# Optimization experiments

Measured on AMD Instinct MI355X. Metric: run time of the kernel, lower is better.

## Reference

```python
import jax, jax.numpy as jnp
import numpy as np
from jax.scipy.special import gammaln

N_NODES = 50000
N_EDGES = 1600000
IN_DIM, H1, H2 = 512, 256, 129  # H2 = hid_dims[-1] + 1 (kappa column)


def setup_inputs() -> dict:
    key = jax.random.key(0)
    k1, k2, k3, k4 = jax.random.split(key, 4)
    x = jax.random.normal(k1, (N_NODES, IN_DIM), dtype=jnp.float32)
    edge_index = jax.random.randint(k2, (2, N_EDGES), 0, N_NODES, dtype=jnp.int32)
    # Glorot-ish init for GCN weights
    W0 = jax.random.normal(k3, (IN_DIM, H1), dtype=jnp.float32) * (1.0 / np.sqrt(IN_DIM))
    W1 = jax.random.normal(k4, (H1, H2), dtype=jnp.float32) * (1.0 / np.sqrt(H1))
    return {"x": x, "edge_index": edge_index, "W0": W0, "W1": W1}


def _gcn_conv(h, W, src, dst, norm, n):
    # PyG GCNConv (bias=False): h' = D^-1/2 (A+I) D^-1/2 (h W)
    h = h @ W
    msg = h[src] * norm[:, None]          # [E+N, F_out]
    return jax.ops.segment_sum(msg, dst, num_segments=n)


def reference(x, edge_index, W0, W1):
    n = x.shape[0]
    loops = jnp.arange(n, dtype=edge_index.dtype)
    src = jnp.concatenate([edge_index[0], loops])
    dst = jnp.concatenate([edge_index[1], loops])
    # symmetric normalization with self-loops (deg >= 1, so rsqrt is safe)
    deg = jax.ops.segment_sum(jnp.ones_like(dst, dtype=x.dtype), dst, num_segments=n)
    dinv = jax.lax.rsqrt(deg)
    norm = dinv[src] * dinv[dst]          # [E+N]

    h = jax.nn.softplus(_gcn_conv(x, W0, src, dst, norm, n))
    # dropout is identity in eval mode (training=False)
    h = jax.nn.softplus(_gcn_conv(h, W1, src, dst, norm, n))

    lbd = h[:, :-1]                       # [N, 128] Weibull scale
    kappa = h[:, -1:] + 0.1               # [N, 1]   Weibull shape
    # deterministic (non-random-encoder / eval) reparameterization:
    # z = lbd * exp(lgamma(1 + 1/kappa))  == E[Weibull(lbd, kappa)]
    z = lbd * jnp.exp(gammaln(1.0 + 1.0 / kappa))
    return z, lbd, kappa
```

## Files before the change

### kernel.cpp

```cpp
#include <hip/hip_runtime.h>
#include <hip/hip_bf16.h>
#include <math.h>


typedef unsigned short ushort_t;
typedef __attribute__((ext_vector_type(8))) short bf16x8;
typedef __attribute__((ext_vector_type(4))) float f32x4;

__device__ __forceinline__ ushort_t f2bf(float f) {
    union { float f; unsigned u; } x; x.f = f;
    unsigned r = x.u + 0x7FFF + ((x.u >> 16) & 1);
    return (ushort_t)(r >> 16);
}
__device__ __forceinline__ float bf2f(ushort_t s) {
    union { unsigned u; float f; } x; x.u = ((unsigned)s) << 16; return x.f;
}

__device__ __forceinline__ void async_copy16(const void* gsrc, void* ldst) {
    __builtin_amdgcn_global_load_lds(
        (const __attribute__((address_space(1))) unsigned int*)gsrc,
        (__attribute__((address_space(3))) unsigned int*)ldst,
        16, 0, 0);
}


__global__ __launch_bounds__(256) void count_kernel(const int* __restrict__ dst,
                                                    int* __restrict__ cnt, int E)
{
    int e = blockIdx.x * blockDim.x + threadIdx.x;
    if (e < E) atomicAdd(&cnt[dst[e]], 1);
}

__global__ __launch_bounds__(1024) void scan_local(const int* __restrict__ cnt,
                                                   int* __restrict__ rowptr,
                                                   float* __restrict__ dinv,
                                                   int* __restrict__ blksum, int N)
{
    __shared__ int wsum[16];
    int tid = threadIdx.x, lane = tid & 63, wid = tid >> 6;
    int i = blockIdx.x * 1024 + tid;
    int v = (i < N) ? cnt[i] : 0;
    if (i < N) dinv[i] = rsqrtf((float)(v + 1));
    int s = v;
#pragma unroll
    for (int off = 1; off < 64; off <<= 1) {
        int t = __shfl_up(s, off, 64);
        if (lane >= off) s += t;
    }
    if (lane == 63) wsum[wid] = s;
    __syncthreads();
    if (tid < 16) {
        int w = wsum[tid];
#pragma unroll
        for (int off = 1; off < 16; off <<= 1) {
            int t = __shfl_up(w, off, 64);
            if (tid >= off) w += t;
        }
        wsum[tid] = w;
    }
    __syncthreads();
    int excl = s - v + (wid ? wsum[wid - 1] : 0);
    if (i < N) rowptr[i] = excl;
    if (tid == 0) blksum[blockIdx.x] = wsum[15];
}

__global__ __launch_bounds__(64) void scan_blk(const int* __restrict__ blksum,
                                               int* __restrict__ blkoff,
                                               int nblk, int* __restrict__ rowptr, int N)
{
    int tid = threadIdx.x;
    int v = (tid < nblk) ? blksum[tid] : 0;
    int s = v;
#pragma unroll
    for (int off = 1; off < 64; off <<= 1) {
        int t = __shfl_up(s, off, 64);
        if (tid >= off) s += t;
    }
    if (tid < nblk) blkoff[tid] = s - v;
    if (tid == nblk - 1) rowptr[N] = s;
}

__global__ __launch_bounds__(256) void scan_add(int* __restrict__ rowptr,
                                                int* __restrict__ cursor,
                                                const int* __restrict__ blkoff, int N)
{
    int i = blockIdx.x * blockDim.x + threadIdx.x;
    if (i < N) {
        int r = rowptr[i] + blkoff[i >> 10];
        rowptr[i] = r;
        cursor[i] = r;
    }
}

__global__ __launch_bounds__(256) void scatter_kernel(const int* __restrict__ src,
                                                      const int* __restrict__ dst,
                                                      int* __restrict__ cursor,
                                                      int* __restrict__ col, int E)
{
    int e = blockIdx.x * blockDim.x + threadIdx.x;
    if (e < E) {
        int d = dst[e];
        int pos = atomicAdd(&cursor[d], 1);
        col[pos] = src[e];
    }
}


__global__ __launch_bounds__(256) void conv_x(const float* __restrict__ x,
                                              ushort_t* __restrict__ Abig,
                                              int M, int M_pad)
{
    int id = blockIdx.x * blockDim.x + threadIdx.x;
    int r = id >> 7, q = id & 127;
    if (r >= M_pad) return;
    float4 v = make_float4(0.f, 0.f, 0.f, 0.f);
    if (r < M) v = *reinterpret_cast<const float4*>(&x[(size_t)r * 512 + q * 4]);
    ushort4 h, l;
    h.x = f2bf(v.x); l.x = f2bf(v.x - bf2f(h.x));
    h.y = f2bf(v.y); l.y = f2bf(v.y - bf2f(h.y));
    h.z = f2bf(v.z); l.z = f2bf(v.z - bf2f(h.z));
    h.w = f2bf(v.w); l.w = f2bf(v.w - bf2f(h.w));
    ushort_t* rowp = Abig + (size_t)r * 1024;
    *reinterpret_cast<ushort4*>(rowp + q * 4)       = h;
    *reinterpret_cast<ushort4*>(rowp + 512 + q * 4) = l;
}

__global__ __launch_bounds__(256) void conv_w0(const float* __restrict__ W0,
                                               ushort_t* __restrict__ BT)
{
    int id = blockIdx.x * blockDim.x + threadIdx.x;
    int k = id & 511, n = id >> 9;
    if (n >= 256) return;
    float v = W0[(size_t)k * 256 + n];
    ushort_t h = f2bf(v);
    ushort_t l = f2bf(v - bf2f(h));
    ushort_t* rowp = BT + (size_t)n * 1536;
    rowp[k] = h; rowp[512 + k] = h; rowp[1024 + k] = l;
}

__global__ __launch_bounds__(256) void conv_w1(const float* __restrict__ W1,
                                               ushort_t* __restrict__ BT,
                                               float* __restrict__ W1col)
{
    int id = blockIdx.x * blockDim.x + threadIdx.x;
    int k = id & 255, n = id >> 8;
    if (n >= 128) return;
    float v = W1[(size_t)k * 129 + n];
    ushort_t h = f2bf(v);
    ushort_t l = f2bf(v - bf2f(h));
    ushort_t* rowp = BT + (size_t)n * 768;
    rowp[k] = h; rowp[256 + k] = h; rowp[512 + k] = l;
    if (n == 0) W1col[k] = W1[(size_t)k * 129 + 128];
}

__global__ __launch_bounds__(256) void gemm_bf16(const ushort_t* __restrict__ A, int lda,
                                                 const ushort_t* __restrict__ BT, int ldbt,
                                                 float* __restrict__ C, int ldc,
                                                 int M, int K, int kwrap)
{
    __shared__ short As[128 * 32];
    __shared__ short Bs[128 * 32];

    int tid  = threadIdx.x;
    int w    = tid >> 6;
    int lane = tid & 63;
    int lm   = lane & 15;
    int lq   = lane >> 4;
    int bm   = blockIdx.x * 128;
    int bn   = blockIdx.y * 128;
    int wr   = (w >> 1) * 64;
    int wc   = (w & 1) * 64;

    f32x4 acc[4][4];
#pragma unroll
    for (int i = 0; i < 4; ++i)
#pragma unroll
        for (int j = 0; j < 4; ++j) acc[i][j] = (f32x4)(0.f);

    int srow = (lane >> 2);
    int scol = (lane & 3) * 16;

    for (int k0 = 0; k0 < K; k0 += 32) {
        int ka = (k0 < kwrap) ? k0 : (k0 - kwrap);
#pragma unroll
        for (int q = 0; q < 2; ++q) {
            int r = w * 32 + q * 16 + srow;
            const char* ga = (const char*)A + ((size_t)(bm + r) * lda + ka) * 2 + scol;
            async_copy16(ga, (char*)As + (size_t)(w * 32 + q * 16) * 64);
        }
#pragma unroll
        for (int q = 0; q < 2; ++q) {
            int r = w * 32 + q * 16 + srow;
            const char* gb = (const char*)BT + ((size_t)(bn + r) * ldbt + k0) * 2 + scol;
            async_copy16(gb, (char*)Bs + (size_t)(w * 32 + q * 16) * 64);
        }
        __syncthreads();

        bf16x8 afr[4], bfr[4];
#pragma unroll
        for (int mi = 0; mi < 4; ++mi)
            afr[mi] = *reinterpret_cast<const bf16x8*>(&As[(wr + mi * 16 + lm) * 32 + lq * 8]);
#pragma unroll
        for (int ni = 0; ni < 4; ++ni)
            bfr[ni] = *reinterpret_cast<const bf16x8*>(&Bs[(wc + ni * 16 + lm) * 32 + lq * 8]);
#pragma unroll
        for (int mi = 0; mi < 4; ++mi)
#pragma unroll
            for (int ni = 0; ni < 4; ++ni)
                acc[mi][ni] = __builtin_amdgcn_mfma_f32_16x16x32_bf16(
                    afr[mi], bfr[ni], acc[mi][ni], 0, 0, 0);
        __syncthreads();
    }

#pragma unroll
    for (int mi = 0; mi < 4; ++mi) {
#pragma unroll
        for (int ni = 0; ni < 4; ++ni) {
            int rbase = bm + wr + mi * 16 + lq * 4;
            int cc    = bn + wc + ni * 16 + lm;
#pragma unroll
            for (int e = 0; e < 4; ++e) {
                int r = rbase + e;
                if (r < M) C[(size_t)r * ldc + cc] = acc[mi][ni][e];
            }
        }
    }
}


__device__ __forceinline__ float softplus_f(float x)
{
    return fmaxf(x, 0.f) + log1pf(expf(-fabsf(x)));
}

__device__ __forceinline__ void fma4(float4& a, float w, const float4& v)
{
    a.x = fmaf(w, v.x, a.x);
    a.y = fmaf(w, v.y, a.y);
    a.z = fmaf(w, v.z, a.z);
    a.w = fmaf(w, v.w, a.w);
}

__device__ __forceinline__ void fma2(float2& a, float w, const float2& v)
{
    a.x = fmaf(w, v.x, a.x);
    a.y = fmaf(w, v.y, a.y);
}

__global__ __launch_bounds__(256) void agg1_kernel(const float* __restrict__ T1,
                                                   const float* __restrict__ dinv,
                                                   const int* __restrict__ rowptr,
                                                   const int* __restrict__ col,
                                                   const float* __restrict__ W1col,
                                                   ushort_t* __restrict__ H1big,
                                                   float* __restrict__ T2k, int N)
{
    int wslot = __builtin_amdgcn_readfirstlane(threadIdx.x >> 6);
    int node  = blockIdx.x * 4 + wslot;
    if (node >= N) return;
    int lane = threadIdx.x & 63;
    float di = dinv[node];
    int beg = rowptr[node], end = rowptr[node + 1];

    float4 acc[4];
#pragma unroll
    for (int i = 0; i < 4; ++i) acc[i] = make_float4(0.f, 0.f, 0.f, 0.f);

    const float* Trow = T1 + (size_t)lane * 4;

    if (beg < end) {
        int last = end - 1;
        int   sc[8]; float wc[8];
#pragma unroll
        for (int j = 0; j < 8; ++j) {
            int idx = beg + j;
            int ss  = col[min(idx, last)];
            sc[j] = ss;
            wc[j] = (idx < end) ? dinv[ss] : 0.f;
        }
        for (int e = beg; e < end; ) {
            float4 vv[8];
#pragma unroll
            for (int j = 0; j < 8; ++j)
                vv[j] = *reinterpret_cast<const float4*>(Trow + (size_t)sc[j] * 256);
            int en = e + 8;
            int   sn[8]; float wn[8];
#pragma unroll
            for (int j = 0; j < 8; ++j) {
                int idx = en + j;
                int ss  = col[min(idx, last)];
                sn[j] = ss;
                wn[j] = (idx < end) ? dinv[ss] : 0.f;
            }
#pragma unroll
            for (int j = 0; j < 8; ++j) fma4(acc[j & 3], wc[j], vv[j]);
#pragma unroll
            for (int j = 0; j < 8; ++j) { sc[j] = sn[j]; wc[j] = wn[j]; }
            e = en;
        }
    }

    float4 self = *reinterpret_cast<const float4*>(Trow + (size_t)node * 256);
    float4 o;
    o.x = softplus_f((acc[0].x + acc[1].x + acc[2].x + acc[3].x + self.x * di) * di);
    o.y = softplus_f((acc[0].y + acc[1].y + acc[2].y + acc[3].y + self.y * di) * di);
    o.z = softplus_f((acc[0].z + acc[1].z + acc[2].z + acc[3].z + self.z * di) * di);
    o.w = softplus_f((acc[0].w + acc[1].w + acc[2].w + acc[3].w + self.w * di) * di);

    ushort4 h, l;
    h.x = f2bf(o.x); l.x = f2bf(o.x - bf2f(h.x));
    h.y = f2bf(o.y); l.y = f2bf(o.y - bf2f(h.y));
    h.z = f2bf(o.z); l.z = f2bf(o.z - bf2f(h.z));
    h.w = f2bf(o.w); l.w = f2bf(o.w - bf2f(h.w));
    ushort_t* rowp = H1big + (size_t)node * 512;
    *reinterpret_cast<ushort4*>(rowp + lane * 4)       = h;
    *reinterpret_cast<ushort4*>(rowp + 256 + lane * 4) = l;

    float4 wv = *reinterpret_cast<const float4*>(&W1col[lane * 4]);
    float tk = o.x * wv.x + o.y * wv.y + o.z * wv.z + o.w * wv.w;
#pragma unroll
    for (int off = 32; off > 0; off >>= 1)
        tk += __shfl_down(tk, off, 64);
    if (lane == 0) T2k[node] = tk;
}

__global__ __launch_bounds__(256) void agg2_kernel(const float* __restrict__ T2,
                                                   const float* __restrict__ T2k,
                                                   const float* __restrict__ dinv,
                                                   const int* __restrict__ rowptr,
                                                   const int* __restrict__ col,
                                                   float* __restrict__ z_out,
                                                   float* __restrict__ lbd_out,
                                                   float* __restrict__ kap_out, int N)
{
    int wslot = __builtin_amdgcn_readfirstlane(threadIdx.x >> 6);
    int node  = blockIdx.x * 4 + wslot;
    if (node >= N) return;
    int lane = threadIdx.x & 63;
    float di = dinv[node];
    int beg = rowptr[node], end = rowptr[node + 1];

    float2 acc[4];
#pragma unroll
    for (int i = 0; i < 4; ++i) acc[i] = make_float2(0.f, 0.f);
    float kk[4] = {0.f, 0.f, 0.f, 0.f};

    const float* Trow = T2 + (size_t)lane * 2;

    if (beg < end) {
        int last = end - 1;
        int   sc[8]; float wc[8]; float tc[8];
#pragma unroll
        for (int j = 0; j < 8; ++j) {
            int idx = beg + j;
            int ss  = col[min(idx, last)];
            sc[j] = ss;
            wc[j] = (idx < end) ? dinv[ss] : 0.f;
            tc[j] = T2k[ss];
        }
        for (int e = beg; e < end; ) {
            float2 vv[8];
#pragma unroll
            for (int j = 0; j < 8; ++j)
                vv[j] = *reinterpret_cast<const float2*>(Trow + (size_t)sc[j] * 128);
            int en = e + 8;
            int   sn[8]; float wn[8]; float tn[8];
#pragma unroll
            for (int j = 0; j < 8; ++j) {
                int idx = en + j;
                int ss  = col[min(idx, last)];
                sn[j] = ss;
                wn[j] = (idx < end) ? dinv[ss] : 0.f;
                tn[j] = T2k[ss];
            }
#pragma unroll
            for (int j = 0; j < 8; ++j) {
                fma2(acc[j & 3], wc[j], vv[j]);
                kk[j & 3] = fmaf(wc[j], tc[j], kk[j & 3]);
            }
#pragma unroll
            for (int j = 0; j < 8; ++j) { sc[j] = sn[j]; wc[j] = wn[j]; tc[j] = tn[j]; }
            e = en;
        }
    }

    float2 self = *reinterpret_cast<const float2*>(Trow + (size_t)node * 128);
    float2 sp;
    sp.x = softplus_f((acc[0].x + acc[1].x + acc[2].x + acc[3].x + self.x * di) * di);
    sp.y = softplus_f((acc[0].y + acc[1].y + acc[2].y + acc[3].y + self.y * di) * di);

    float ak = ((kk[0] + kk[1] + kk[2] + kk[3]) + T2k[node] * di) * di;
    float kv = softplus_f(ak) + 0.1f;
    float g  = expf(lgammaf(1.0f + 1.0f / kv));
    if (lane == 0) kap_out[node] = kv;

    size_t o = (size_t)node * 128 + lane * 2;
    float2 zv = make_float2(sp.x * g, sp.y * g);
    *reinterpret_cast<float2*>(&lbd_out[o]) = sp;
    *reinterpret_cast<float2*>(&z_out[o])   = zv;
}

extern "C" void kernel_launch(void* const* d_in, const int* in_sizes, int n_in,
                              void* d_out, int out_size, void* d_ws, size_t ws_size,
                              hipStream_t stream)
{
    const float* x  = (const float*)d_in[0];
    const int*   ei = (const int*)d_in[1];
    const float* W0 = (const float*)d_in[2];
    const float* W1 = (const float*)d_in[3];

    const int N = in_sizes[0] / 512;
    const int E = in_sizes[1] / 2;
    const int* src = ei;
    const int* dst = ei + E;

    const int mblocks = (N + 127) / 128;
    const int M_pad   = mblocks * 128;
    const int nchunk  = (N + 1023) / 1024;

    char* w = (char*)d_ws;
    size_t off = 0;
    auto take = [&](size_t bytes) -> void* {
        void* p = (void*)(w + off);
        off = (off + bytes + 255) & ~(size_t)255;
        return p;
    };
    int*      cnt    = (int*)take((size_t)N * 4);
    int*      rowptr = (int*)take((size_t)(N + 1) * 4);
    int*      cursor = (int*)take((size_t)N * 4);
    float*    dinv   = (float*)take((size_t)N * 4);
    int*      col    = (int*)take((size_t)E * 4);
    int*      blksum = (int*)take(64 * 4);
    int*      blkoff = (int*)take(64 * 4);
    ushort_t* W0bigT = (ushort_t*)take((size_t)256 * 1536 * 2);
    ushort_t* W1bigT = (ushort_t*)take((size_t)128 * 768 * 2);
    float*    W1col  = (float*)take((size_t)256 * 4);
    float*    T2k    = (float*)take((size_t)N * 4);
    float*    T1     = (float*)take((size_t)N * 256 * 4);
    float*    T2     = T1;
    ushort_t* Abig   = (ushort_t*)take((size_t)M_pad * 1024 * 2);
    ushort_t* H1big  = Abig;

    float* z_out   = (float*)d_out;
    float* lbd_out = z_out + (size_t)N * 128;
    float* kap_out = lbd_out + (size_t)N * 128;

    hipMemsetAsync(cnt, 0, (size_t)N * 4, stream);
    count_kernel<<<(E + 255) / 256, 256, 0, stream>>>(dst, cnt, E);
    scan_local<<<nchunk, 1024, 0, stream>>>(cnt, rowptr, dinv, blksum, N);
    scan_blk<<<1, 64, 0, stream>>>(blksum, blkoff, nchunk, rowptr, N);
    scan_add<<<(N + 255) / 256, 256, 0, stream>>>(rowptr, cursor, blkoff, N);
    scatter_kernel<<<(E + 255) / 256, 256, 0, stream>>>(src, dst, cursor, col, E);

    conv_x<<<(M_pad * 128) / 256, 256, 0, stream>>>(x, Abig, N, M_pad);
    conv_w0<<<(256 * 512) / 256, 256, 0, stream>>>(W0, W0bigT);
    conv_w1<<<(128 * 256) / 256, 256, 0, stream>>>(W1, W1bigT, W1col);

    dim3 g1(mblocks, 2);
    gemm_bf16<<<g1, 256, 0, stream>>>(Abig, 1024, W0bigT, 1536, T1, 256, N, 1536, 1024);

    agg1_kernel<<<(N + 3) / 4, 256, 0, stream>>>(T1, dinv, rowptr, col, W1col, H1big, T2k, N);

    dim3 g2(mblocks, 1);
    gemm_bf16<<<g2, 256, 0, stream>>>(H1big, 512, W1bigT, 768, T2, 128, N, 768, 512);

    agg2_kernel<<<(N + 3) / 4, 256, 0, stream>>>(T2, T2k, dinv, rowptr, col,
                                                 z_out, lbd_out, kap_out, N);
}
```

Before: 838.0 us.

## Bucket CSR neighbor lists by source-node range for locality in aggregation

Builds the CSR with a two-level key (destination, source bucket of 2048 nodes), so each node's neighbor list comes out roughly sorted by source index. The aggregation kernels then gather T1/T2 rows in a more cache-friendly order. The cost is a 25x larger count/scan array (N*25 entries), an extra scan level, and a separate dinv kernel. The count and cursor arrays are borrowed from the T1 buffer, which is still free at that point in the pipeline.

After: 847.3 us. About the same (+1.1%).

```diff
diff --git a/kernel.cpp b/kernel.cpp
--- a/kernel.cpp
+++ b/kernel.cpp
@@ -6,6 +6,9 @@
 typedef unsigned short ushort_t;
 typedef __attribute__((ext_vector_type(8))) short bf16x8;
 typedef __attribute__((ext_vector_type(4))) float f32x4;
+
+#define NB 25
+#define BSHIFT 11
 
 __device__ __forceinline__ ushort_t f2bf(float f) {
     union { float f; unsigned u; } x; x.f = f;
@@ -24,23 +27,22 @@
 }
 
 
-__global__ __launch_bounds__(256) void count_kernel(const int* __restrict__ dst,
-                                                    int* __restrict__ cnt, int E)
+__global__ __launch_bounds__(256) void count2_kernel(const int* __restrict__ src,
+                                                     const int* __restrict__ dst,
+                                                     int* __restrict__ cnt2, int E)
 {
     int e = blockIdx.x * blockDim.x + threadIdx.x;
-    if (e < E) atomicAdd(&cnt[dst[e]], 1);
+    if (e < E) atomicAdd(&cnt2[dst[e] * NB + (src[e] >> BSHIFT)], 1);
 }
 
 __global__ __launch_bounds__(1024) void scan_local(const int* __restrict__ cnt,
-                                                   int* __restrict__ rowptr,
-                                                   float* __restrict__ dinv,
+                                                   int* __restrict__ outp,
                                                    int* __restrict__ blksum, int N)
 {
     __shared__ int wsum[16];
     int tid = threadIdx.x, lane = tid & 63, wid = tid >> 6;
     int i = blockIdx.x * 1024 + tid;
     int v = (i < N) ? cnt[i] : 0;
-    if (i < N) dinv[i] = rsqrtf((float)(v + 1));
     int s = v;
 #pragma unroll
     for (int off = 1; off < 64; off <<= 1) {
@@ -60,13 +62,13 @@
     }
     __syncthreads();
     int excl = s - v + (wid ? wsum[wid - 1] : 0);
-    if (i < N) rowptr[i] = excl;
+    if (i < N) outp[i] = excl;
     if (tid == 0) blksum[blockIdx.x] = wsum[15];
 }
 
 __global__ __launch_bounds__(64) void scan_blk(const int* __restrict__ blksum,
                                                int* __restrict__ blkoff,
-                                               int nblk, int* __restrict__ rowptr, int N)
+                                               int nblk, int* __restrict__ endp, int LEN)
 {
     int tid = threadIdx.x;
     int v = (tid < nblk) ? blksum[tid] : 0;
@@ -77,31 +79,43 @@
         if (tid >= off) s += t;
     }
     if (tid < nblk) blkoff[tid] = s - v;
-    if (tid == nblk - 1) rowptr[N] = s;
-}
-
-__global__ __launch_bounds__(256) void scan_add(int* __restrict__ rowptr,
-                                                int* __restrict__ cursor,
-                                                const int* __restrict__ blkoff, int N)
+    if (tid == nblk - 1) endp[LEN] = s;
+}
+
+__global__ __launch_bounds__(256) void final_add(int* __restrict__ R2,
+                                                 int* __restrict__ cursor2,
+                                                 const int* __restrict__ bs1p,
+                                                 const int* __restrict__ bo2, int LEN)
+{
+    int i = blockIdx.x * blockDim.x + threadIdx.x;
+    if (i < LEN) {
+        int r = R2[i] + bs1p[i >> 10] + bo2[i >> 20];
+        R2[i] = r;
+        cursor2[i] = r;
+    }
+}
+
+__global__ __launch_bounds__(256) void dinv_kernel(const int* __restrict__ R2,
+                                                   float* __restrict__ dinv, int N)
 {
     int i = blockIdx.x * blockDim.x + threadIdx.x;
     if (i < N) {
-        int r = rowptr[i] + blkoff[i >> 10];
-        rowptr[i] = r;
-        cursor[i] = r;
-    }
-}
-
-__global__ __launch_bounds__(256) void scatter_kernel(const int* __restrict__ src,
-                                                      const int* __restrict__ dst,
-                                                      int* __restrict__ cursor,
-                                                      int* __restrict__ col, int E)
+        int beg = R2[i * NB];
+        int end = R2[(i + 1) * NB];
+        dinv[i] = rsqrtf((float)(end - beg + 1));
+    }
+}
+
+__global__ __launch_bounds__(256) void scatter2_kernel(const int* __restrict__ src,
+                                                       const int* __restrict__ dst,
+                                                       int* __restrict__ cursor2,
+                                                       int* __restrict__ col, int E)
 {
     int e = blockIdx.x * blockDim.x + threadIdx.x;
     if (e < E) {
-        int d = dst[e];
-        int pos = atomicAdd(&cursor[d], 1);
-        col[pos] = src[e];
+        int d = dst[e], s = src[e];
+        int pos = atomicAdd(&cursor2[d * NB + (s >> BSHIFT)], 1);
+        col[pos] = s;
     }
 }
 
@@ -249,7 +263,7 @@
 
 __global__ __launch_bounds__(256) void agg1_kernel(const float* __restrict__ T1,
                                                    const float* __restrict__ dinv,
-                                                   const int* __restrict__ rowptr,
+                                                   const int* __restrict__ R2,
                                                    const int* __restrict__ col,
                                                    const float* __restrict__ W1col,
                                                    ushort_t* __restrict__ H1big,
@@ -260,7 +274,7 @@
     if (node >= N) return;
     int lane = threadIdx.x & 63;
     float di = dinv[node];
-    int beg = rowptr[node], end = rowptr[node + 1];
+    int beg = R2[node * NB], end = R2[(node + 1) * NB];
 
     float4 acc[4];
 #pragma unroll
@@ -327,7 +341,7 @@
 __global__ __launch_bounds__(256) void agg2_kernel(const float* __restrict__ T2,
                                                    const float* __restrict__ T2k,
                                                    const float* __restrict__ dinv,
-                                                   const int* __restrict__ rowptr,
+                                                   const int* __restrict__ R2,
                                                    const int* __restrict__ col,
                                                    float* __restrict__ z_out,
                                                    float* __restrict__ lbd_out,
@@ -338,7 +352,7 @@
     if (node >= N) return;
     int lane = threadIdx.x & 63;
     float di = dinv[node];
-    int beg = rowptr[node], end = rowptr[node + 1];
+    int beg = R2[node * NB], end = R2[(node + 1) * NB];
 
     float2 acc[4];
 #pragma unroll
@@ -416,7 +430,9 @@
 
     const int mblocks = (N + 127) / 128;
     const int M_pad   = mblocks * 128;
-    const int nchunk  = (N + 1023) / 1024;
+    const int LEN     = N * NB;
+    const int nblk1   = (LEN + 1023) / 1024;
+    const int nblk2   = (nblk1 + 1023) / 1024;
 
     char* w = (char*)d_ws;
     size_t off = 0;
@@ -425,13 +441,13 @@
         off = (off + bytes + 255) & ~(size_t)255;
         return p;
     };
-    int*      cnt    = (int*)take((size_t)N * 4);
-    int*      rowptr = (int*)take((size_t)(N + 1) * 4);
-    int*      cursor = (int*)take((size_t)N * 4);
+    int*      R2     = (int*)take((size_t)(LEN + 1) * 4);
     float*    dinv   = (float*)take((size_t)N * 4);
     int*      col    = (int*)take((size_t)E * 4);
-    int*      blksum = (int*)take(64 * 4);
-    int*      blkoff = (int*)take(64 * 4);
+    int*      bs1    = (int*)take((size_t)1280 * 4);
+    int*      bs1p   = (int*)take((size_t)1280 * 4);
+    int*      bs2    = (int*)take((size_t)64 * 4);
+    int*      bo2    = (int*)take((size_t)64 * 4);
     ushort_t* W0bigT = (ushort_t*)take((size_t)256 * 1536 * 2);
     ushort_t* W1bigT = (ushort_t*)take((size_t)128 * 768 * 2);
     float*    W1col  = (float*)take((size_t)256 * 4);
@@ -441,16 +457,21 @@
     ushort_t* Abig   = (ushort_t*)take((size_t)M_pad * 1024 * 2);
     ushort_t* H1big  = Abig;
 
+    int* cnt2    = (int*)T1;
+    int* cursor2 = (int*)((char*)T1 + (size_t)16 * 1024 * 1024);
+
     float* z_out   = (float*)d_out;
     float* lbd_out = z_out + (size_t)N * 128;
     float* kap_out = lbd_out + (size_t)N * 128;
 
-    hipMemsetAsync(cnt, 0, (size_t)N * 4, stream);
-    count_kernel<<<(E + 255) / 256, 256, 0, stream>>>(dst, cnt, E);
-    scan_local<<<nchunk, 1024, 0, stream>>>(cnt, rowptr, dinv, blksum, N);
-    scan_blk<<<1, 64, 0, stream>>>(blksum, blkoff, nchunk, rowptr, N);
-    scan_add<<<(N + 255) / 256, 256, 0, stream>>>(rowptr, cursor, blkoff, N);
-    scatter_kernel<<<(E + 255) / 256, 256, 0, stream>>>(src, dst, cursor, col, E);
+    hipMemsetAsync(cnt2, 0, (size_t)LEN * 4, stream);
+    count2_kernel<<<(E + 255) / 256, 256, 0, stream>>>(src, dst, cnt2, E);
+    scan_local<<<nblk1, 1024, 0, stream>>>(cnt2, R2, bs1, LEN);
+    scan_local<<<nblk2, 1024, 0, stream>>>(bs1, bs1p, bs2, nblk1);
+    scan_blk<<<1, 64, 0, stream>>>(bs2, bo2, nblk2, R2, LEN);
+    final_add<<<(LEN + 255) / 256, 256, 0, stream>>>(R2, cursor2, bs1p, bo2, LEN);
+    dinv_kernel<<<(N + 255) / 256, 256, 0, stream>>>(R2, dinv, N);
+    scatter2_kernel<<<(E + 255) / 256, 256, 0, stream>>>(src, dst, cursor2, col, E);
 
     conv_x<<<(M_pad * 128) / 256, 256, 0, stream>>>(x, Abig, N, M_pad);
     conv_w0<<<(256 * 512) / 256, 256, 0, stream>>>(W0, W0bigT);
@@ -459,11 +480,11 @@
     dim3 g1(mblocks, 2);
     gemm_bf16<<<g1, 256, 0, stream>>>(Abig, 1024, W0bigT, 1536, T1, 256, N, 1536, 1024);
 
-    agg1_kernel<<<(N + 3) / 4, 256, 0, stream>>>(T1, dinv, rowptr, col, W1col, H1big, T2k, N);
+    agg1_kernel<<<(N + 3) / 4, 256, 0, stream>>>(T1, dinv, R2, col, W1col, H1big, T2k, N);
 
     dim3 g2(mblocks, 1);
     gemm_bf16<<<g2, 256, 0, stream>>>(H1big, 512, W1bigT, 768, T2, 128, N, 768, 512);
 
-    agg2_kernel<<<(N + 3) / 4, 256, 0, stream>>>(T2, T2k, dinv, rowptr, col,
+    agg2_kernel<<<(N + 3) / 4, 256, 0, stream>>>(T2, T2k, dinv, R2, col,
                                                  z_out, lbd_out, kap_out, N);
 }
```
